# Kernel optimization log

Measured on AMD Instinct MI355X. Metric: run time of the kernel, lower is better.

The kernel has to match this reference:

```python
import jax, jax.numpy as jnp
import numpy as np

MAX_SH_DEGREE = 3
NUM_BASES = (MAX_SH_DEGREE + 1) ** 2  # 16


def eval_sh_bases_fast(dirs):
    """SH bases up to degree 3 for unit directions [..., 3] -> [..., 16].
    Matches gsplat's _eval_sh_bases_fast constants/order."""
    x, y, z = dirs[..., 0], dirs[..., 1], dirs[..., 2]
    z2 = z * z
    fTmp0B = -1.092548430592079 * z
    fC1 = x * x - y * y
    fS1 = 2.0 * x * y
    fTmp0C = -2.285228997322329 * z2 + 0.4570457994644658
    fTmp1B = 1.445305721320277 * z
    fC2 = x * fC1 - y * fS1
    fS2 = x * fS1 + y * fC1
    ones = jnp.full_like(x, 0.2820947917738781)
    return jnp.stack([
        ones,
        -0.48860251190292 * y,
        0.48860251190292 * z,
        -0.48860251190292 * x,
        0.5462742152960395 * fS1,
        fTmp0B * y,
        0.9461746957575601 * z2 - 0.3153915652525201,
        fTmp0B * x,
        0.5462742152960395 * fC1,
        -0.5900435899266435 * fS2,
        fTmp1B * fS1,
        fTmp0C * y,
        z * (1.865881662950577 * z2 - 1.119528997770346),
        fTmp0C * x,
        fTmp1B * fC1,
        -0.5900435899266435 * fC2,
    ], axis=-1)


def setup_inputs() -> dict:
    key = jax.random.key(0)
    ks = jax.random.split(key, 10)
    C, N, F, E, W = 4, 250000, 32, 16, 128
    D_IN = E + F + NUM_BASES  # 64
    return {
        "features": jax.random.normal(ks[0], (N, F), jnp.float32),
        "dirs": jax.random.normal(ks[1], (C, N, 3), jnp.float32),
        "embed_table": jax.random.normal(ks[2], (1000, E), jnp.float32) * 0.1,
        "W0": jax.random.normal(ks[3], (D_IN, W), jnp.float32) / np.sqrt(D_IN),
        "b0": jax.random.normal(ks[4], (W,), jnp.float32) * 0.01,
        "W1": jax.random.normal(ks[5], (W, W), jnp.float32) / np.sqrt(W),
        "b1": jax.random.normal(ks[6], (W,), jnp.float32) * 0.01,
        "W2": jax.random.normal(ks[7], (W, 3), jnp.float32) / np.sqrt(W),
        "b2": jax.random.normal(ks[8], (3,), jnp.float32) * 0.01,
        "embed_ids": jax.random.randint(ks[9], (C,), 0, 1000, jnp.int64 if jax.config.jax_enable_x64 else jnp.int32),
        "sh_degree": 3,
    }


def reference(features, dirs, embed_table, W0, b0, W1, b1, W2, b2, embed_ids, sh_degree):
    C, N = dirs.shape[:2]
    E = embed_table.shape[1]
    F_dim = features.shape[1]
    # camera embeddings broadcast over splats
    emb = embed_table[embed_ids]                                   # [C, E]
    emb = jnp.broadcast_to(emb[:, None, :], (C, N, E))
    feats = jnp.broadcast_to(features[None, :, :], (C, N, F_dim))
    # F.normalize(dirs, dim=-1): divide by norm clamped at eps=1e-12
    norm = jnp.linalg.norm(dirs, axis=-1, keepdims=True)
    nd = dirs / jnp.maximum(norm, 1e-12)
    nb_use = (sh_degree + 1) ** 2  # static python int
    sh = eval_sh_bases_fast(nd)                                    # [C, N, 16]
    if nb_use < NUM_BASES:  # zero bases beyond requested degree
        mask = (jnp.arange(NUM_BASES) < nb_use).astype(sh.dtype)
        sh = sh * mask
    x = jnp.concatenate([emb, feats, sh], axis=-1)                 # [C, N, 64]
    h = jax.nn.relu(x @ W0 + b0)
    h = jax.nn.relu(h @ W1 + b1)
    return h @ W2 + b2                                             # [C, N, 3]
```

## Files before the change

kernel.cpp:

```cpp
#include <hip/hip_runtime.h>
#include <cstdint>
#include <cstddef>

typedef _Float16 half8 __attribute__((ext_vector_type(8)));
typedef __fp16 fp16x2 __attribute__((ext_vector_type(2)));
typedef float floatx16 __attribute__((ext_vector_type(16)));
typedef unsigned uint2v __attribute__((ext_vector_type(2)));


__global__ void vdc_prep_kernel(const float* __restrict__ W0,
                                const float* __restrict__ W1,
                                const float* __restrict__ W2,
                                const float* __restrict__ b0,
                                const float* __restrict__ b1,
                                const float* __restrict__ b2,
                                const float* __restrict__ emb_tab,
                                const int* __restrict__ embed_ids,
                                int C,
                                _Float16* __restrict__ ws) {
    int i = blockIdx.x * 256 + threadIdx.x;
    int w0end = C * 8192;
    int w1end = w0end + 18432;
    int w2end = w1end + 4608;
    float v = 0.0f;
    if (i < w0end) {
        int c = i >> 13, r = i & 8191;
        int ci = r >> 9, l = (r >> 3) & 63, ii = r & 7;
        int mt = ci >> 2, ks = ci & 3;
        int j  = mt * 32 + (l & 31);
        int kk = ks * 16 + (l >> 5) * 8 + ii;
        if (kk < 48) v = W0[(16 + kk) * 128 + j];
        else if (kk == 48) {
            int id = embed_ids[c];
            v = b0[j];
            #pragma unroll
            for (int e = 0; e < 16; ++e)
                v += emb_tab[(size_t)id * 16 + e] * W0[e * 128 + j];
        }
        ws[i] = (_Float16)v;
    } else if (i < w1end) {
        int r = i - w0end;
        int ci = r >> 9, l = (r >> 3) & 63, ii = r & 7;
        int mt = ci / 9, ks = ci - mt * 9;
        int j  = mt * 32 + (l & 31);
        int kk = ks * 16 + (l >> 5) * 8 + ii;
        if (kk < 128) v = W1[kk * 128 + j];
        else if (kk == 128) v = b1[j];
        ws[i] = (_Float16)v;
    } else if (i < w2end) {
        int r = i - w1end;
        int ks = r >> 9, l = (r >> 3) & 63, ii = r & 7;
        int o  = l & 31;
        int kk = ks * 16 + (l >> 5) * 8 + ii;
        if (o < 3) {
            if (kk < 128) v = W2[kk * 3 + o];
            else if (kk == 128) v = b2[o];
        }
        ws[i] = (_Float16)v;
    }
}

union U4 { unsigned u[4]; half8 h; };

__device__ __forceinline__ unsigned pkr(float a, float b) {
    union { fp16x2 h; unsigned u; } x;
    x.h = __builtin_amdgcn_cvt_pkrtz(a, b);
    return x.u;
}

__device__ __forceinline__ unsigned pkrelu(float a, float b) {
    union { fp16x2 h; unsigned u; } x;
    x.h = __builtin_amdgcn_cvt_pkrtz(a, b);
    fp16x2 z = {(__fp16)0.0f, (__fp16)0.0f};
    x.h = __builtin_elementwise_max(x.h, z);
    return x.u;
}

__device__ __forceinline__ floatx16 zero16() {
    floatx16 z;
    #pragma unroll
    for (int r = 0; r < 16; ++r) z[r] = 0.0f;
    return z;
}

__device__ __forceinline__ void transition(const floatx16& a, int hl,
                                           half8& lo, half8& hi) {
    unsigned p0 = pkrelu(a[0],  a[1]);
    unsigned p1 = pkrelu(a[2],  a[3]);
    unsigned p2 = pkrelu(a[4],  a[5]);
    unsigned p3 = pkrelu(a[6],  a[7]);
    unsigned p4 = pkrelu(a[8],  a[9]);
    unsigned p5 = pkrelu(a[10], a[11]);
    unsigned p6 = pkrelu(a[12], a[13]);
    unsigned p7 = pkrelu(a[14], a[15]);
    U4 L, H;
#if __has_builtin(__builtin_amdgcn_permlane32_swap)
    uint2v s02 = __builtin_amdgcn_permlane32_swap(p0, p2, false, false);
    uint2v s13 = __builtin_amdgcn_permlane32_swap(p1, p3, false, false);
    uint2v s46 = __builtin_amdgcn_permlane32_swap(p4, p6, false, false);
    uint2v s57 = __builtin_amdgcn_permlane32_swap(p5, p7, false, false);
    L.u[0] = s02[0]; L.u[1] = s13[0]; L.u[2] = s02[1]; L.u[3] = s13[1];
    H.u[0] = s46[0]; H.u[1] = s57[0]; H.u[2] = s46[1]; H.u[3] = s57[1];
    (void)hl;
#else
    unsigned r0 = __shfl_xor(hl ? p0 : p2, 32);
    unsigned r1 = __shfl_xor(hl ? p1 : p3, 32);
    unsigned r2 = __shfl_xor(hl ? p4 : p6, 32);
    unsigned r3 = __shfl_xor(hl ? p5 : p7, 32);
    L.u[0] = hl ? r0 : p0;
    L.u[1] = hl ? r1 : p1;
    L.u[2] = hl ? p2 : r0;
    L.u[3] = hl ? p3 : r1;
    H.u[0] = hl ? r2 : p4;
    H.u[1] = hl ? r3 : p5;
    H.u[2] = hl ? p6 : r2;
    H.u[3] = hl ? p7 : r3;
#endif
    lo = L.h; hi = H.h;
}

__device__ __forceinline__ void build_bfrags(
    const float* __restrict__ feats, const float* __restrict__ dirs,
    size_t cN, int n, int hl, int nbu,
    half8& o0, half8& o1, half8& o2)
{
    const float* fp = feats + (size_t)n * 32 + hl * 8;
    float4 f0 = *(const float4*)(fp);
    float4 f1 = *(const float4*)(fp + 4);
    float4 f2 = *(const float4*)(fp + 16);
    float4 f3 = *(const float4*)(fp + 20);
    U4 u0, u1;
    u0.u[0] = pkr(f0.x, f0.y); u0.u[1] = pkr(f0.z, f0.w);
    u0.u[2] = pkr(f1.x, f1.y); u0.u[3] = pkr(f1.z, f1.w);
    u1.u[0] = pkr(f2.x, f2.y); u1.u[1] = pkr(f2.z, f2.w);
    u1.u[2] = pkr(f3.x, f3.y); u1.u[3] = pkr(f3.z, f3.w);
    o0 = u0.h; o1 = u1.h;

    const float* dp = dirs + (cN + n) * 3;
    float dx = dp[0], dy = dp[1], dz = dp[2];
    float nrm = sqrtf(dx * dx + dy * dy + dz * dz);
    float inv = 1.0f / fmaxf(nrm, 1e-12f);
    float x = dx * inv, y = dy * inv, z = dz * inv;

    float z2     = z * z;
    float fTmp0B = -1.092548430592079f * z;
    float fC1    = x * x - y * y;
    float fS1    = 2.0f * x * y;
    float fTmp0C = -2.285228997322329f * z2 + 0.4570457994644658f;
    float fTmp1B = 1.445305721320277f * z;
    float fC2    = x * fC1 - y * fS1;
    float fS2    = x * fS1 + y * fC1;

    float sh[16];
    sh[0]  = 0.2820947917738781f;
    sh[1]  = -0.48860251190292f * y;
    sh[2]  = 0.48860251190292f * z;
    sh[3]  = -0.48860251190292f * x;
    sh[4]  = 0.5462742152960395f * fS1;
    sh[5]  = fTmp0B * y;
    sh[6]  = 0.9461746957575601f * z2 - 0.3153915652525201f;
    sh[7]  = fTmp0B * x;
    sh[8]  = 0.5462742152960395f * fC1;
    sh[9]  = -0.5900435899266435f * fS2;
    sh[10] = fTmp1B * fS1;
    sh[11] = fTmp0C * y;
    sh[12] = z * (1.865881662950577f * z2 - 1.119528997770346f);
    sh[13] = fTmp0C * x;
    sh[14] = fTmp1B * fC1;
    sh[15] = -0.5900435899266435f * fC2;
    #pragma unroll
    for (int i = 0; i < 16; ++i) if (i >= nbu) sh[i] = 0.0f;

    float s0 = hl ? sh[8]  : sh[0];
    float s1 = hl ? sh[9]  : sh[1];
    float s2 = hl ? sh[10] : sh[2];
    float s3 = hl ? sh[11] : sh[3];
    float s4 = hl ? sh[12] : sh[4];
    float s5 = hl ? sh[13] : sh[5];
    float s6 = hl ? sh[14] : sh[6];
    float s7 = hl ? sh[15] : sh[7];
    U4 u2;
    u2.u[0] = pkr(s0, s1); u2.u[1] = pkr(s2, s3);
    u2.u[2] = pkr(s4, s5); u2.u[3] = pkr(s6, s7);
    o2 = u2.h;
}

#define MFMA(a, b, c) __builtin_amdgcn_mfma_f32_32x32x16_f16((a), (b), (c), 0, 0, 0)
#define LDF(off) (*(const half8*)(fr + (off)))
#define GW2(ch) (*(const half8*)(w2p + (ch) * 512 + lane * 8))

#define L0_MT(MT, HA0, HA1, HB0, HB1)                                    \
    do {                                                                 \
        floatx16 ca = zacc;                                              \
        floatx16 cb = zacc;                                              \
        half8 t0 = LDF(((MT) * 4 + 0) * 1024);                           \
        ca = MFMA(t0, ax0, ca); cb = MFMA(t0, bx0, cb);                  \
        half8 t1 = LDF(((MT) * 4 + 1) * 1024);                           \
        ca = MFMA(t1, ax1, ca); cb = MFMA(t1, bx1, cb);                  \
        half8 t2 = LDF(((MT) * 4 + 2) * 1024);                           \
        ca = MFMA(t2, ax2, ca); cb = MFMA(t2, bx2, cb);                  \
        half8 t3 = LDF(((MT) * 4 + 3) * 1024);                           \
        ca = MFMA(t3, bbias, ca); cb = MFMA(t3, bbias, cb);              \
        transition(ca, hl, HA0, HA1);                                    \
        transition(cb, hl, HB0, HB1);                                    \
    } while (0)

#define L1_KS(MT, KS, HA, HB)                                            \
    do {                                                                 \
        half8 q = LDF(16384 + ((MT) * 9 + (KS)) * 1024);                 \
        ca = MFMA(q, HA, ca); cb = MFMA(q, HB, cb);                      \
    } while (0)

#define L1_MT(MT)                                                        \
    do {                                                                 \
        floatx16 ca = zacc;                                              \
        floatx16 cb = zacc;                                              \
        L1_KS(MT, 0, ha0, hb0);                                          \
        L1_KS(MT, 1, ha1, hb1);                                          \
        L1_KS(MT, 2, ha2, hb2);                                          \
        L1_KS(MT, 3, ha3, hb3);                                          \
        L1_KS(MT, 4, ha4, hb4);                                          \
        L1_KS(MT, 5, ha5, hb5);                                          \
        L1_KS(MT, 6, ha6, hb6);                                          \
        L1_KS(MT, 7, ha7, hb7);                                          \
        L1_KS(MT, 8, bbias, bbias);                                      \
        half8 w2a = GW2(2 * (MT) + 0);                                   \
        half8 w2b = GW2(2 * (MT) + 1);                                   \
        half8 g0, g1;                                                    \
        transition(ca, hl, g0, g1);                                      \
        acc3a = MFMA(w2a, g0, acc3a); acc3a = MFMA(w2b, g1, acc3a);      \
        transition(cb, hl, g0, g1);                                      \
        acc3b = MFMA(w2a, g0, acc3b); acc3b = MFMA(w2b, g1, acc3b);      \
    } while (0)

__global__ __launch_bounds__(256, 3) void vdc_mlp_kernel(
    const float* __restrict__ feats,
    const float* __restrict__ dirs,
    const int* __restrict__ sh_deg_p,
    const _Float16* __restrict__ ws,
    float* __restrict__ out,
    int N, int C)
{
    __shared__ uint4 arena[3328];
    char* lds = (char*)arena;

    const int tid   = threadIdx.x;
    const int c     = blockIdx.y;
    const int w     = tid >> 6;
    const int lane  = tid & 63;
    const int ln    = lane & 31;
    const int hl    = lane >> 5;
    const int base  = blockIdx.x * 256 + w * 64;

    const _Float16* w2p = ws + (size_t)C * 8192 + 18432;

    {
        const uint4* srcA = (const uint4*)(ws + (size_t)c * 8192);
        const uint4* srcB = (const uint4*)(ws + (size_t)C * 8192);
        #pragma unroll
        for (int it = 0; it < 13; ++it) {
            int idx = it * 256 + tid;
            arena[idx] = (idx < 1024) ? srcA[idx] : srcB[idx - 1024];
        }
    }

    half8 bbias;
    {
        U4 ub;
        ub.u[0] = hl ? 0u : 0x00003C00u;
        ub.u[1] = 0u; ub.u[2] = 0u; ub.u[3] = 0u;
        bbias = ub.h;
    }
    int deg = sh_deg_p[0];
    int nbu = (deg + 1) * (deg + 1);
    int na = base + ln;      if (na >= N) na = N - 1;
    int nb = base + 32 + ln; if (nb >= N) nb = N - 1;
    half8 ax0, ax1, ax2, bx0, bx1, bx2;
    build_bfrags(feats, dirs, (size_t)c * N, na, hl, nbu, ax0, ax1, ax2);
    build_bfrags(feats, dirs, (size_t)c * N, nb, hl, nbu, bx0, bx1, bx2);

    const floatx16 zacc = zero16();

    __syncthreads();

    const char* fr = lds + lane * 16;

    half8 ha0, ha1, ha2, ha3, ha4, ha5, ha6, ha7;
    half8 hb0, hb1, hb2, hb3, hb4, hb5, hb6, hb7;
    L0_MT(0, ha0, ha1, hb0, hb1);
    L0_MT(1, ha2, ha3, hb2, hb3);
    L0_MT(2, ha4, ha5, hb4, hb5);
    L0_MT(3, ha6, ha7, hb6, hb7);

    floatx16 acc3a = zacc;
    floatx16 acc3b = zacc;
    L1_MT(0);
    L1_MT(1);
    L1_MT(2);
    L1_MT(3);
    {
        half8 ab = GW2(8);
        acc3a = MFMA(ab, bbias, acc3a);
        acc3b = MFMA(ab, bbias, acc3b);
    }

    if (hl == 0) {
        int nn = base + ln;
        if (nn < N) {
            float* op = out + ((size_t)c * N + nn) * 3;
            op[0] = acc3a[0];
            op[1] = acc3a[1];
            op[2] = acc3a[2];
        }
        nn = base + 32 + ln;
        if (nn < N) {
            float* op = out + ((size_t)c * N + nn) * 3;
            op[0] = acc3b[0];
            op[1] = acc3b[1];
            op[2] = acc3b[2];
        }
    }
}

extern "C" void kernel_launch(void* const* d_in, const int* in_sizes, int n_in,
                              void* d_out, int out_size, void* d_ws, size_t ws_size,
                              hipStream_t stream) {
    const float* feats   = (const float*)d_in[0];
    const float* dirs    = (const float*)d_in[1];
    const float* emb_tab = (const float*)d_in[2];
    const float* W0      = (const float*)d_in[3];
    const float* b0      = (const float*)d_in[4];
    const float* W1      = (const float*)d_in[5];
    const float* b1      = (const float*)d_in[6];
    const float* W2      = (const float*)d_in[7];
    const float* b2      = (const float*)d_in[8];
    const int*   eids    = (const int*)d_in[9];
    const int*   shd     = (const int*)d_in[10];
    float* outp          = (float*)d_out;

    int N = in_sizes[0] / 32;
    int C = in_sizes[9];

    _Float16* wsh = (_Float16*)d_ws;

    int ws_elems = C * 8192 + 23040;
    vdc_prep_kernel<<<(ws_elems + 255) / 256, 256, 0, stream>>>(
        W0, W1, W2, b0, b1, b2, emb_tab, eids, C, wsh);

    dim3 grid((N + 255) / 256, C);
    vdc_mlp_kernel<<<grid, 256, 0, stream>>>(
        feats, dirs, shd, wsh, outp, N, C);
}
```

Baseline: 148.1 us.

## Process two point tiles per block and software-pipeline layer-1 weight LDS loads

Each block now handles 512 points in two passes, so the LDS weight staging and barrier cost is spread over twice the work and the grid is halved. The layer-1 inner loop is rewritten to keep three weight fragments in flight, issuing LDS reads ahead of the MFMAs that consume them, and the W2 fragments are loaded at the start of each tile. The trade-off is fewer blocks, which means less parallelism and tail imbalance, plus higher register pressure under launch_bounds(256,3) that could cause spills.

```diff
diff --git a/kernel.cpp b/kernel.cpp
--- a/kernel.cpp
+++ b/kernel.cpp
@@ -205,27 +205,30 @@
         transition(cb, hl, HB0, HB1);                                    \
     } while (0)
 
-#define L1_KS(MT, KS, HA, HB)                                            \
-    do {                                                                 \
-        half8 q = LDF(16384 + ((MT) * 9 + (KS)) * 1024);                 \
-        ca = MFMA(q, HA, ca); cb = MFMA(q, HB, cb);                      \
-    } while (0)
-
 #define L1_MT(MT)                                                        \
     do {                                                                 \
+        half8 w2a = GW2(2 * (MT) + 0);                                   \
+        half8 w2b = GW2(2 * (MT) + 1);                                   \
         floatx16 ca = zacc;                                              \
         floatx16 cb = zacc;                                              \
-        L1_KS(MT, 0, ha0, hb0);                                          \
-        L1_KS(MT, 1, ha1, hb1);                                          \
-        L1_KS(MT, 2, ha2, hb2);                                          \
-        L1_KS(MT, 3, ha3, hb3);                                          \
-        L1_KS(MT, 4, ha4, hb4);                                          \
-        L1_KS(MT, 5, ha5, hb5);                                          \
-        L1_KS(MT, 6, ha6, hb6);                                          \
-        L1_KS(MT, 7, ha7, hb7);                                          \
-        L1_KS(MT, 8, bbias, bbias);                                      \
-        half8 w2a = GW2(2 * (MT) + 0);                                   \
-        half8 w2b = GW2(2 * (MT) + 1);                                   \
+        half8 p0 = LDF(16384 + ((MT) * 9 + 0) * 1024);                   \
+        half8 p1 = LDF(16384 + ((MT) * 9 + 1) * 1024);                   \
+        half8 p2 = LDF(16384 + ((MT) * 9 + 2) * 1024);                   \
+        ca = MFMA(p0, ha0, ca); cb = MFMA(p0, hb0, cb);                  \
+        p0 = LDF(16384 + ((MT) * 9 + 3) * 1024);                         \
+        ca = MFMA(p1, ha1, ca); cb = MFMA(p1, hb1, cb);                  \
+        p1 = LDF(16384 + ((MT) * 9 + 4) * 1024);                         \
+        ca = MFMA(p2, ha2, ca); cb = MFMA(p2, hb2, cb);                  \
+        p2 = LDF(16384 + ((MT) * 9 + 5) * 1024);                         \
+        ca = MFMA(p0, ha3, ca); cb = MFMA(p0, hb3, cb);                  \
+        p0 = LDF(16384 + ((MT) * 9 + 6) * 1024);                         \
+        ca = MFMA(p1, ha4, ca); cb = MFMA(p1, hb4, cb);                  \
+        p1 = LDF(16384 + ((MT) * 9 + 7) * 1024);                         \
+        ca = MFMA(p2, ha5, ca); cb = MFMA(p2, hb5, cb);                  \
+        p2 = LDF(16384 + ((MT) * 9 + 8) * 1024);                         \
+        ca = MFMA(p0, ha6, ca); cb = MFMA(p0, hb6, cb);                  \
+        ca = MFMA(p1, ha7, ca); cb = MFMA(p1, hb7, cb);                  \
+        ca = MFMA(p2, bbias, ca); cb = MFMA(p2, bbias, cb);              \
         half8 g0, g1;                                                    \
         transition(ca, hl, g0, g1);                                      \
         acc3a = MFMA(w2a, g0, acc3a); acc3a = MFMA(w2b, g1, acc3a);      \
@@ -250,7 +253,6 @@
     const int lane  = tid & 63;
     const int ln    = lane & 31;
     const int hl    = lane >> 5;
-    const int base  = blockIdx.x * 256 + w * 64;
 
     const _Float16* w2p = ws + (size_t)C * 8192 + 18432;
 
@@ -273,51 +275,56 @@
     }
     int deg = sh_deg_p[0];
     int nbu = (deg + 1) * (deg + 1);
-    int na = base + ln;      if (na >= N) na = N - 1;
-    int nb = base + 32 + ln; if (nb >= N) nb = N - 1;
-    half8 ax0, ax1, ax2, bx0, bx1, bx2;
-    build_bfrags(feats, dirs, (size_t)c * N, na, hl, nbu, ax0, ax1, ax2);
-    build_bfrags(feats, dirs, (size_t)c * N, nb, hl, nbu, bx0, bx1, bx2);
-
     const floatx16 zacc = zero16();
-
-    __syncthreads();
-
     const char* fr = lds + lane * 16;
 
-    half8 ha0, ha1, ha2, ha3, ha4, ha5, ha6, ha7;
-    half8 hb0, hb1, hb2, hb3, hb4, hb5, hb6, hb7;
-    L0_MT(0, ha0, ha1, hb0, hb1);
-    L0_MT(1, ha2, ha3, hb2, hb3);
-    L0_MT(2, ha4, ha5, hb4, hb5);
-    L0_MT(3, ha6, ha7, hb6, hb7);
-
-    floatx16 acc3a = zacc;
-    floatx16 acc3b = zacc;
-    L1_MT(0);
-    L1_MT(1);
-    L1_MT(2);
-    L1_MT(3);
-    {
-        half8 ab = GW2(8);
-        acc3a = MFMA(ab, bbias, acc3a);
-        acc3b = MFMA(ab, bbias, acc3b);
-    }
-
-    if (hl == 0) {
-        int nn = base + ln;
-        if (nn < N) {
-            float* op = out + ((size_t)c * N + nn) * 3;
-            op[0] = acc3a[0];
-            op[1] = acc3a[1];
-            op[2] = acc3a[2];
-        }
-        nn = base + 32 + ln;
-        if (nn < N) {
-            float* op = out + ((size_t)c * N + nn) * 3;
-            op[0] = acc3b[0];
-            op[1] = acc3b[1];
-            op[2] = acc3b[2];
+    bool synced = false;
+    #pragma unroll
+    for (int pass = 0; pass < 2; ++pass) {
+        const int base = blockIdx.x * 512 + pass * 256 + w * 64;
+
+        int na = base + ln;      if (na >= N) na = N - 1;
+        int nb = base + 32 + ln; if (nb >= N) nb = N - 1;
+        half8 ax0, ax1, ax2, bx0, bx1, bx2;
+        build_bfrags(feats, dirs, (size_t)c * N, na, hl, nbu, ax0, ax1, ax2);
+        build_bfrags(feats, dirs, (size_t)c * N, nb, hl, nbu, bx0, bx1, bx2);
+
+        if (!synced) { __syncthreads(); synced = true; }
+
+        half8 ha0, ha1, ha2, ha3, ha4, ha5, ha6, ha7;
+        half8 hb0, hb1, hb2, hb3, hb4, hb5, hb6, hb7;
+        L0_MT(0, ha0, ha1, hb0, hb1);
+        L0_MT(1, ha2, ha3, hb2, hb3);
+        L0_MT(2, ha4, ha5, hb4, hb5);
+        L0_MT(3, ha6, ha7, hb6, hb7);
+
+        floatx16 acc3a = zacc;
+        floatx16 acc3b = zacc;
+        L1_MT(0);
+        L1_MT(1);
+        L1_MT(2);
+        L1_MT(3);
+        {
+            half8 ab = GW2(8);
+            acc3a = MFMA(ab, bbias, acc3a);
+            acc3b = MFMA(ab, bbias, acc3b);
+        }
+
+        if (hl == 0) {
+            int nn = base + ln;
+            if (nn < N) {
+                float* op = out + ((size_t)c * N + nn) * 3;
+                op[0] = acc3a[0];
+                op[1] = acc3a[1];
+                op[2] = acc3a[2];
+            }
+            nn = base + 32 + ln;
+            if (nn < N) {
+                float* op = out + ((size_t)c * N + nn) * 3;
+                op[0] = acc3b[0];
+                op[1] = acc3b[1];
+                op[2] = acc3b[2];
+            }
         }
     }
 }
@@ -347,7 +354,7 @@
     vdc_prep_kernel<<<(ws_elems + 255) / 256, 256, 0, stream>>>(
         W0, W1, W2, b0, b1, b2, emb_tab, eids, C, wsh);
 
-    dim3 grid((N + 255) / 256, C);
+    dim3 grid((N + 511) / 512, C);
     vdc_mlp_kernel<<<grid, 256, 0, stream>>>(
         feats, dirs, shd, wsh, outp, N, C);
 }
```

New measurement: 148.9 us. No clear change (+0.5%).
